# Kernel optimization log

Hardware: AMD Instinct MI355X
Metric: run time of the kernel (lower is better)

The kernel has to match this reference:

```python
import jax, jax.numpy as jnp
import numpy as np

B, N = 4096, 1024


def setup_inputs() -> dict:
    key = jax.random.key(0)
    k1, k2 = jax.random.split(key)
    cors = 0.1 * jax.random.normal(k1, (B, N, 3), dtype=jnp.float32)  # predicted correspondences/offsets
    p_src = jax.random.normal(k2, (B, N, 3), dtype=jnp.float32)       # source point cloud
    return {"cors": cors, "p_src": p_src}


def reference(cors, p_src):
    # p_pred = p_src + cors  (target points implied by correspondences)
    p_pred = p_src + cors
    # centroids over the point dimension: [B, 1, 3]
    src_centroid = jnp.mean(p_src, axis=1, keepdims=True)
    pred_centroid = jnp.mean(p_pred, axis=1, keepdims=True)
    src_trans = p_src - src_centroid
    pred_trans = p_pred - pred_centroid
    # 3x3 cross-covariance per batch: h = src_trans^T @ pred_trans  -> [B, 3, 3]
    h = jnp.einsum('bnd,bne->bde', src_trans, pred_trans)
    # tf.linalg.svd returns s, u, v with h = u diag(s) v^T; jnp returns u, s, vh with vh = v^T
    u, s, vh = jnp.linalg.svd(h, full_matrices=False)
    # r_est = v @ u^T = (u @ vh)^T
    r_est = jnp.swapaxes(jnp.matmul(u, vh), -1, -2)  # [B, 3, 3]
    # t_est = -r_est @ src_centroid^T + pred_centroid^T  -> [B, 3, 1]
    t_est = -jnp.matmul(r_est, jnp.swapaxes(src_centroid, -1, -2)) + jnp.swapaxes(pred_centroid, -1, -2)
    g_top = jnp.concatenate([r_est, t_est], axis=2)  # [B, 3, 4]
    last_row = jnp.broadcast_to(
        jnp.array([[[0.0, 0.0, 0.0, 1.0]]], dtype=g_top.dtype), (g_top.shape[0], 1, 4)
    )
    return jnp.concatenate([g_top, last_row], axis=1)  # [B, 4, 4]
```

## Files before the change

### kernel.cpp

```cpp
#include <hip/hip_runtime.h>


constexpr int NPTS    = 1024;
constexpr int THREADS = 256;
constexpr int NF4     = NPTS * 3 / 4;

__global__ __launch_bounds__(THREADS) void svd_layer_kernel(
    const float* __restrict__ cors,
    const float* __restrict__ p_src,
    float* __restrict__ out)
{
    __shared__ float4 lds_s[NF4];
    __shared__ float4 lds_c[NF4];
    __shared__ float  red[4][15];

    const int b = blockIdx.x;
    const int t = threadIdx.x;
    const int wave = t >> 6, lane = t & 63;

    const float4* s4 = reinterpret_cast<const float4*>(p_src) + (size_t)b * NF4;
    const float4* c4 = reinterpret_cast<const float4*>(cors)  + (size_t)b * NF4;

    float4 a0 = s4[t], a1 = s4[t + 256], a2 = s4[t + 512];
    float4 b0 = c4[t], b1 = c4[t + 256], b2 = c4[t + 512];
    lds_s[t] = a0; lds_s[t + 256] = a1; lds_s[t + 512] = a2;
    lds_c[t] = b0; lds_c[t + 256] = b1; lds_c[t + 512] = b2;
    __syncthreads();

    const float4 t0 = lds_s[t*3+0], t1 = lds_s[t*3+1], t2 = lds_s[t*3+2];
    const float4 u0 = lds_c[t*3+0], u1 = lds_c[t*3+1], u2 = lds_c[t*3+2];

    const float sx[4] = {t0.x, t0.w, t1.z, t2.y};
    const float sy[4] = {t0.y, t1.x, t1.w, t2.z};
    const float sz[4] = {t0.z, t1.y, t2.x, t2.w};
    const float px[4] = {sx[0]+u0.x, sx[1]+u0.w, sx[2]+u1.z, sx[3]+u2.y};
    const float py[4] = {sy[0]+u0.y, sy[1]+u1.x, sy[2]+u1.w, sy[3]+u2.z};
    const float pz[4] = {sz[0]+u0.z, sz[1]+u1.y, sz[2]+u2.x, sz[3]+u2.w};

    float acc[15];
    #pragma unroll
    for (int i = 0; i < 15; ++i) acc[i] = 0.f;
    #pragma unroll
    for (int k = 0; k < 4; ++k) {
        acc[0]  += sx[k]; acc[1]  += sy[k]; acc[2]  += sz[k];
        acc[3]  += px[k]; acc[4]  += py[k]; acc[5]  += pz[k];
        acc[6]  += sx[k]*px[k]; acc[7]  += sx[k]*py[k]; acc[8]  += sx[k]*pz[k];
        acc[9]  += sy[k]*px[k]; acc[10] += sy[k]*py[k]; acc[11] += sy[k]*pz[k];
        acc[12] += sz[k]*px[k]; acc[13] += sz[k]*py[k]; acc[14] += sz[k]*pz[k];
    }

    #pragma unroll
    for (int off = 32; off > 0; off >>= 1) {
        #pragma unroll
        for (int i = 0; i < 15; ++i) acc[i] += __shfl_down(acc[i], off, 64);
    }

    if (lane == 0) {
        #pragma unroll
        for (int i = 0; i < 15; ++i) red[wave][i] = acc[i];
    }
    __syncthreads();
    if (t != 0) return;

    float S[15];
    #pragma unroll
    for (int i = 0; i < 15; ++i)
        S[i] = red[0][i] + red[1][i] + red[2][i] + red[3][i];

    const float invN = 1.0f / (float)NPTS;
    const float cs[3] = {S[0]*invN, S[1]*invN, S[2]*invN};
    const float cp[3] = {S[3]*invN, S[4]*invN, S[5]*invN};

    float Hm[3][3];
    #pragma unroll
    for (int i = 0; i < 3; ++i)
        #pragma unroll
        for (int j = 0; j < 3; ++j)
            Hm[i][j] = S[6 + i*3 + j] - (float)NPTS * cs[i] * cp[j];

    float K[3][3];
    #pragma unroll
    for (int i = 0; i < 3; ++i)
        #pragma unroll
        for (int j = 0; j < 3; ++j)
            K[i][j] = Hm[0][i]*Hm[0][j] + Hm[1][i]*Hm[1][j] + Hm[2][i]*Hm[2][j];

    const float tr3 = (K[0][0] + K[1][1] + K[2][2]) * (1.0f/3.0f);
    const float is  = 1.0f / fmaxf(tr3, 1e-30f);

    float Y[3][3], Z[3][3];
    #pragma unroll
    for (int i = 0; i < 3; ++i)
        #pragma unroll
        for (int j = 0; j < 3; ++j) {
            Y[i][j] = K[i][j] * is;
            Z[i][j] = (i == j) ? 1.0f : 0.0f;
        }

    #pragma unroll
    for (int it = 0; it < 6; ++it) {
        float W[3][3];
        #pragma unroll
        for (int i = 0; i < 3; ++i)
            #pragma unroll
            for (int j = 0; j < 3; ++j) {
                float w = Z[i][0]*Y[0][j] + Z[i][1]*Y[1][j] + Z[i][2]*Y[2][j];
                W[i][j] = ((i == j) ? 1.5f : 0.0f) - 0.5f * w;
            }
        float Yn[3][3], Zn[3][3];
        #pragma unroll
        for (int i = 0; i < 3; ++i)
            #pragma unroll
            for (int j = 0; j < 3; ++j) {
                Yn[i][j] = Y[i][0]*W[0][j] + Y[i][1]*W[1][j] + Y[i][2]*W[2][j];
                Zn[i][j] = W[i][0]*Z[0][j] + W[i][1]*Z[1][j] + W[i][2]*Z[2][j];
            }
        #pragma unroll
        for (int i = 0; i < 3; ++i)
            #pragma unroll
            for (int j = 0; j < 3; ++j) { Y[i][j] = Yn[i][j]; Z[i][j] = Zn[i][j]; }
    }

    const float rs = rsqrtf(fmaxf(tr3, 1e-30f));
    float R[3][3];
    #pragma unroll
    for (int i = 0; i < 3; ++i)
        #pragma unroll
        for (int j = 0; j < 3; ++j)
            R[i][j] = (Z[i][0]*Hm[j][0] + Z[i][1]*Hm[j][1] + Z[i][2]*Hm[j][2]) * rs;

    const float tx = cp[0] - (R[0][0]*cs[0] + R[0][1]*cs[1] + R[0][2]*cs[2]);
    const float ty = cp[1] - (R[1][0]*cs[0] + R[1][1]*cs[1] + R[1][2]*cs[2]);
    const float tz = cp[2] - (R[2][0]*cs[0] + R[2][1]*cs[1] + R[2][2]*cs[2]);

    float4* o4 = reinterpret_cast<float4*>(out + (size_t)b * 16);
    o4[0] = make_float4(R[0][0], R[0][1], R[0][2], tx);
    o4[1] = make_float4(R[1][0], R[1][1], R[1][2], ty);
    o4[2] = make_float4(R[2][0], R[2][1], R[2][2], tz);
    o4[3] = make_float4(0.f, 0.f, 0.f, 1.f);
}

extern "C" void kernel_launch(void* const* d_in, const int* in_sizes, int n_in,
                              void* d_out, int out_size, void* d_ws, size_t ws_size,
                              hipStream_t stream)
{
    const float* cors  = (const float*)d_in[0];
    const float* p_src = (const float*)d_in[1];
    float* out = (float*)d_out;
    const int B = in_sizes[0] / (NPTS * 3);
    hipLaunchKernelGGL(svd_layer_kernel, dim3(B), dim3(THREADS), 0, stream,
                       cors, p_src, out);
}
```

Before: 118.7 us.

## Process four batches per block with register prefetch of the next batch

Each block now handles four consecutive batch elements in a loop. While the current batch is reduced out of LDS, the next batch's float4 loads are issued into registers. The per-batch sums go to a small shared array, and four threads then run the serial 3x3 polar/SVD tail in parallel. The aim is to hide global load latency and spread the single-thread tail over more useful work per block, at the cost of launching a quarter as many blocks and therefore exposing less parallelism across the GPU.

```diff
diff --git a/kernel.cpp b/kernel.cpp
--- a/kernel.cpp
+++ b/kernel.cpp
@@ -4,6 +4,7 @@
 constexpr int NPTS    = 1024;
 constexpr int THREADS = 256;
 constexpr int NF4     = NPTS * 3 / 4;
+constexpr int BPB     = 4;
 
 __global__ __launch_bounds__(THREADS) void svd_layer_kernel(
     const float* __restrict__ cors,
@@ -13,59 +14,72 @@
     __shared__ float4 lds_s[NF4];
     __shared__ float4 lds_c[NF4];
     __shared__ float  red[4][15];
+    __shared__ float  allS[BPB][15];
 
-    const int b = blockIdx.x;
     const int t = threadIdx.x;
     const int wave = t >> 6, lane = t & 63;
+    const int b0 = blockIdx.x * BPB;
 
-    const float4* s4 = reinterpret_cast<const float4*>(p_src) + (size_t)b * NF4;
-    const float4* c4 = reinterpret_cast<const float4*>(cors)  + (size_t)b * NF4;
+    const float4* s4 = reinterpret_cast<const float4*>(p_src) + (size_t)b0 * NF4;
+    const float4* c4 = reinterpret_cast<const float4*>(cors)  + (size_t)b0 * NF4;
 
     float4 a0 = s4[t], a1 = s4[t + 256], a2 = s4[t + 512];
-    float4 b0 = c4[t], b1 = c4[t + 256], b2 = c4[t + 512];
-    lds_s[t] = a0; lds_s[t + 256] = a1; lds_s[t + 512] = a2;
-    lds_c[t] = b0; lds_c[t + 256] = b1; lds_c[t + 512] = b2;
-    __syncthreads();
+    float4 d0 = c4[t], d1 = c4[t + 256], d2 = c4[t + 512];
 
-    const float4 t0 = lds_s[t*3+0], t1 = lds_s[t*3+1], t2 = lds_s[t*3+2];
-    const float4 u0 = lds_c[t*3+0], u1 = lds_c[t*3+1], u2 = lds_c[t*3+2];
+    for (int k = 0; k < BPB; ++k) {
+        lds_s[t] = a0; lds_s[t + 256] = a1; lds_s[t + 512] = a2;
+        lds_c[t] = d0; lds_c[t + 256] = d1; lds_c[t + 512] = d2;
+        __syncthreads();
 
-    const float sx[4] = {t0.x, t0.w, t1.z, t2.y};
-    const float sy[4] = {t0.y, t1.x, t1.w, t2.z};
-    const float sz[4] = {t0.z, t1.y, t2.x, t2.w};
-    const float px[4] = {sx[0]+u0.x, sx[1]+u0.w, sx[2]+u1.z, sx[3]+u2.y};
-    const float py[4] = {sy[0]+u0.y, sy[1]+u1.x, sy[2]+u1.w, sy[3]+u2.z};
-    const float pz[4] = {sz[0]+u0.z, sz[1]+u1.y, sz[2]+u2.x, sz[3]+u2.w};
+        if (k + 1 < BPB) {
+            const float4* sn = s4 + (size_t)(k + 1) * NF4;
+            const float4* cn = c4 + (size_t)(k + 1) * NF4;
+            a0 = sn[t]; a1 = sn[t + 256]; a2 = sn[t + 512];
+            d0 = cn[t]; d1 = cn[t + 256]; d2 = cn[t + 512];
+        }
 
-    float acc[15];
-    #pragma unroll
-    for (int i = 0; i < 15; ++i) acc[i] = 0.f;
-    #pragma unroll
-    for (int k = 0; k < 4; ++k) {
-        acc[0]  += sx[k]; acc[1]  += sy[k]; acc[2]  += sz[k];
-        acc[3]  += px[k]; acc[4]  += py[k]; acc[5]  += pz[k];
-        acc[6]  += sx[k]*px[k]; acc[7]  += sx[k]*py[k]; acc[8]  += sx[k]*pz[k];
-        acc[9]  += sy[k]*px[k]; acc[10] += sy[k]*py[k]; acc[11] += sy[k]*pz[k];
-        acc[12] += sz[k]*px[k]; acc[13] += sz[k]*py[k]; acc[14] += sz[k]*pz[k];
+        const float4 t0 = lds_s[t*3+0], t1 = lds_s[t*3+1], t2 = lds_s[t*3+2];
+        const float4 u0 = lds_c[t*3+0], u1 = lds_c[t*3+1], u2 = lds_c[t*3+2];
+
+        const float sx[4] = {t0.x, t0.w, t1.z, t2.y};
+        const float sy[4] = {t0.y, t1.x, t1.w, t2.z};
+        const float sz[4] = {t0.z, t1.y, t2.x, t2.w};
+        const float px[4] = {sx[0]+u0.x, sx[1]+u0.w, sx[2]+u1.z, sx[3]+u2.y};
+        const float py[4] = {sy[0]+u0.y, sy[1]+u1.x, sy[2]+u1.w, sy[3]+u2.z};
+        const float pz[4] = {sz[0]+u0.z, sz[1]+u1.y, sz[2]+u2.x, sz[3]+u2.w};
+
+        float acc[15];
+        #pragma unroll
+        for (int i = 0; i < 15; ++i) acc[i] = 0.f;
+        #pragma unroll
+        for (int q = 0; q < 4; ++q) {
+            acc[0]  += sx[q]; acc[1]  += sy[q]; acc[2]  += sz[q];
+            acc[3]  += px[q]; acc[4]  += py[q]; acc[5]  += pz[q];
+            acc[6]  += sx[q]*px[q]; acc[7]  += sx[q]*py[q]; acc[8]  += sx[q]*pz[q];
+            acc[9]  += sy[q]*px[q]; acc[10] += sy[q]*py[q]; acc[11] += sy[q]*pz[q];
+            acc[12] += sz[q]*px[q]; acc[13] += sz[q]*py[q]; acc[14] += sz[q]*pz[q];
+        }
+
+        #pragma unroll
+        for (int off = 32; off > 0; off >>= 1) {
+            #pragma unroll
+            for (int i = 0; i < 15; ++i) acc[i] += __shfl_down(acc[i], off, 64);
+        }
+
+        if (lane == 0) {
+            #pragma unroll
+            for (int i = 0; i < 15; ++i) red[wave][i] = acc[i];
+        }
+        __syncthreads();
+        if (t < 15) allS[k][t] = red[0][t] + red[1][t] + red[2][t] + red[3][t];
     }
 
-    #pragma unroll
-    for (int off = 32; off > 0; off >>= 1) {
-        #pragma unroll
-        for (int i = 0; i < 15; ++i) acc[i] += __shfl_down(acc[i], off, 64);
-    }
-
-    if (lane == 0) {
-        #pragma unroll
-        for (int i = 0; i < 15; ++i) red[wave][i] = acc[i];
-    }
     __syncthreads();
-    if (t != 0) return;
+    if (t >= BPB) return;
 
     float S[15];
     #pragma unroll
-    for (int i = 0; i < 15; ++i)
-        S[i] = red[0][i] + red[1][i] + red[2][i] + red[3][i];
+    for (int i = 0; i < 15; ++i) S[i] = allS[t][i];
 
     const float invN = 1.0f / (float)NPTS;
     const float cs[3] = {S[0]*invN, S[1]*invN, S[2]*invN};
@@ -133,7 +147,7 @@
     const float ty = cp[1] - (R[1][0]*cs[0] + R[1][1]*cs[1] + R[1][2]*cs[2]);
     const float tz = cp[2] - (R[2][0]*cs[0] + R[2][1]*cs[1] + R[2][2]*cs[2]);
 
-    float4* o4 = reinterpret_cast<float4*>(out + (size_t)b * 16);
+    float4* o4 = reinterpret_cast<float4*>(out + (size_t)(b0 + t) * 16);
     o4[0] = make_float4(R[0][0], R[0][1], R[0][2], tx);
     o4[1] = make_float4(R[1][0], R[1][1], R[1][2], ty);
     o4[2] = make_float4(R[2][0], R[2][1], R[2][2], tz);
@@ -148,6 +162,7 @@
     const float* p_src = (const float*)d_in[1];
     float* out = (float*)d_out;
     const int B = in_sizes[0] / (NPTS * 3);
-    hipLaunchKernelGGL(svd_layer_kernel, dim3(B), dim3(THREADS), 0, stream,
+    const int grid = B / BPB;
+    hipLaunchKernelGGL(svd_layer_kernel, dim3(grid), dim3(THREADS), 0, stream,
                        cors, p_src, out);
 }
```

After: 118.8 us. No clear change (+0.1%).
